# Performance work log

Measured on AMD Instinct MI355X. Metric: run time of the kernel, lower is better.

Reference implementation:

```python
import jax, jax.numpy as jnp
import numpy as np

N_NODES = 50000
N_EDGES = 800000
IN_F, HID, OUT_F = 256, 128, 8
N_LAYERS = 3
N_GRAPHS = 256
NEG_SLOPE = 0.2  # PyG GATConv default negative_slope


def setup_inputs() -> dict:
    key = jax.random.key(0)
    ks = jax.random.split(key, 16)
    inp = {
        "x": jax.random.normal(ks[0], (N_NODES, IN_F), dtype=jnp.float32),
        "edge_index": jax.random.randint(ks[1], (2, N_EDGES), 0, N_NODES, dtype=jnp.int64),
        "edge_attr": jax.random.normal(ks[2], (N_EDGES, 8), dtype=jnp.float32),
        "batch": jnp.sort(jax.random.randint(ks[3], (N_NODES,), 0, N_GRAPHS, dtype=jnp.int64)),
    }
    # Per-layer GATConv params (heads=1): lin weight, att_src, att_dst, bias.
    dims = [(IN_F, HID), (HID, HID), (HID, HID)]
    for l, (di, do) in enumerate(dims):
        s = 1.0 / np.sqrt(di)
        inp[f"W{l}"] = jax.random.uniform(ks[4 + l], (di, do), jnp.float32, -s, s)
        inp[f"a_src{l}"] = jax.random.normal(ks[7 + l], (do,), jnp.float32) * 0.1
        inp[f"a_dst{l}"] = jax.random.normal(ks[10 + l], (do,), jnp.float32) * 0.1
        inp[f"b{l}"] = jnp.zeros((do,), jnp.float32)
    s = 1.0 / np.sqrt(HID)
    inp["lin_w"] = jax.random.uniform(ks[13], (HID, OUT_F), jnp.float32, -s, s)
    inp["lin_b"] = jnp.zeros((OUT_F,), jnp.float32)
    return inp


def _segment_softmax(logits, seg, num_segments):
    m = jax.ops.segment_max(logits, seg, num_segments=num_segments)
    e = jnp.exp(logits - m[seg])
    s = jax.ops.segment_sum(e, seg, num_segments=num_segments)
    return e / s[seg]


def _gat_layer(x, src, dst, W, a_src, a_dst, b):
    h = x @ W                              # [N, H]
    alpha_s = h @ a_src                    # [N]
    alpha_d = h @ a_dst                    # [N]
    logits = jax.nn.leaky_relu(alpha_s[src] + alpha_d[dst], NEG_SLOPE)  # [E]
    alpha = _segment_softmax(logits, dst, N_NODES)                      # [E]
    out = jax.ops.segment_sum(alpha[:, None] * h[src], dst, num_segments=N_NODES)
    return out + b


def reference(x, edge_index, edge_attr, batch,
              W0, a_src0, a_dst0, b0,
              W1, a_src1, a_dst1, b1,
              W2, a_src2, a_dst2, b2,
              lin_w, lin_b):
    src, dst = edge_index[0], edge_index[1]
    # is_edge_attr=False: edge_attr unused, matching the else-branch.
    h = _gat_layer(x, src, dst, W0, a_src0, a_dst0, b0)
    h = jax.nn.relu(h)
    h = _gat_layer(h, src, dst, W1, a_src1, a_dst1, b1)
    h = jax.nn.relu(h)
    h = _gat_layer(h, src, dst, W2, a_src2, a_dst2, b2)  # last layer: no relu
    # global_mean_pool
    sums = jax.ops.segment_sum(h, batch, num_segments=N_GRAPHS)
    cnt = jax.ops.segment_sum(jnp.ones((N_NODES,), h.dtype), batch, num_segments=N_GRAPHS)
    pooled = sums / jnp.maximum(cnt, 1.0)[:, None]
    # Dropout is identity in eval mode.
    return pooled @ lin_w + lin_b  # logits [G, OUT_F]
```

## Files before the change

kernel.cpp:

```cpp
#include <hip/hip_runtime.h>
#include <cstdint>
#include <cstddef>

#define N_NODES_C  50000
#define N_EDGES_C  800000
#define IN_F_C     256
#define HID_C      128
#define N_GRAPHS_C 256
#define NEG_SLOPE_C 0.2f
#define SCAN_NB    ((N_NODES_C + 255) / 256)
#define POOL_SPLIT 8

typedef _Float16 f16x8 __attribute__((ext_vector_type(8)));
typedef float    f32x4 __attribute__((ext_vector_type(4)));

__global__ void hist_kernel(const int* __restrict__ dst, int* __restrict__ deg, int E) {
    int e = blockIdx.x * blockDim.x + threadIdx.x;
    if (e < E) atomicAdd(&deg[dst[e]], 1);
}

__global__ __launch_bounds__(256) void scan1_kernel(const int* __restrict__ deg,
                                                    int* __restrict__ bsum, int n) {
    int i = blockIdx.x * 256 + threadIdx.x;
    int lane = threadIdx.x & 63;
    int w = threadIdx.x >> 6;
    int v = (i < n) ? deg[i] : 0;
    #pragma unroll
    for (int off = 32; off >= 1; off >>= 1) v += __shfl_xor(v, off);
    __shared__ int ws_[4];
    if (lane == 0) ws_[w] = v;
    __syncthreads();
    if (threadIdx.x == 0) bsum[blockIdx.x] = ws_[0] + ws_[1] + ws_[2] + ws_[3];
}

__global__ __launch_bounds__(256) void scan2_kernel(int* __restrict__ bsum, int nb) {
    int t = threadIdx.x;
    int lane = t & 63;
    int w = t >> 6;
    int orig = (t < nb) ? bsum[t] : 0;
    int v = orig;
    #pragma unroll
    for (int off = 1; off < 64; off <<= 1) {
        int u = __shfl_up(v, off);
        if (lane >= off) v += u;
    }
    __shared__ int wsum[4];
    if (lane == 63) wsum[w] = v;
    __syncthreads();
    int add = 0;
    for (int i = 0; i < w; ++i) add += wsum[i];
    if (t < nb) bsum[t] = v + add - orig;
}

__global__ __launch_bounds__(256) void scan3_kernel(const int* __restrict__ deg,
                                                    const int* __restrict__ boff,
                                                    int* __restrict__ row_start,
                                                    int* __restrict__ cursor, int n) {
    int i = blockIdx.x * 256 + threadIdx.x;
    int lane = threadIdx.x & 63;
    int w = threadIdx.x >> 6;
    int d = (i < n) ? deg[i] : 0;
    int v = d;
    #pragma unroll
    for (int off = 1; off < 64; off <<= 1) {
        int u = __shfl_up(v, off);
        if (lane >= off) v += u;
    }
    __shared__ int wsum[4];
    if (lane == 63) wsum[w] = v;
    __syncthreads();
    int add = boff[blockIdx.x];
    for (int k = 0; k < w; ++k) add += wsum[k];
    int excl = v - d + add;
    if (i < n) {
        row_start[i] = excl;
        cursor[i] = excl;
        if (i == n - 1) row_start[n] = excl + d;
    }
}

__global__ void scatter_kernel(const int* __restrict__ src, const int* __restrict__ dst, int E,
                               int* __restrict__ cursor, int* __restrict__ csr_src) {
    int e = blockIdx.x * blockDim.x + threadIdx.x;
    if (e < E) {
        int pos = atomicAdd(&cursor[dst[e]], 1);
        csr_src[pos] = src[e];
    }
}

__global__ void convert_w_kernel(const float* __restrict__ W,
                                 _Float16* __restrict__ wt_hi,
                                 _Float16* __restrict__ wt_lo, int K) {
    int id = blockIdx.x * 256 + threadIdx.x;
    if (id >= K * 128) return;
    int c = id & 127;
    int k = id >> 7;
    float w = W[(size_t)k * 128 + c];
    _Float16 h = (_Float16)w;
    _Float16 l = (_Float16)(w - (float)h);
    wt_hi[(size_t)c * K + k] = h;
    wt_lo[(size_t)c * K + k] = l;
}

template <int K, bool RELU>
__global__ __launch_bounds__(256) void gemm_mfma_kernel(
    const float* __restrict__ X,
    const _Float16* __restrict__ WTh, const _Float16* __restrict__ WTl,
    const float* __restrict__ a_src, const float* __restrict__ a_dst,
    _Float16* __restrict__ Hh, float* __restrict__ alpha_s, float* __restrict__ alpha_d,
    int n_rows)
{
    constexpr int NS = K / 32;
    __shared__ _Float16 XsH[2][64 * 32];
    __shared__ _Float16 XsL[2][64 * 32];
    __shared__ float aps[4][64];
    __shared__ float apd[4][64];

    const int t = threadIdx.x;
    const int row0 = blockIdx.x * 64;
    const int lane = t & 63;
    const int wv = t >> 6;
    const int l15 = lane & 15;
    const int l4 = lane >> 4;
    const int wcol = wv * 32;

    const int sr = t >> 2;
    const int skg = t & 3;
    const int sgrow = row0 + sr;
    const int sslot = skg ^ (sr & 3);
    const int sldsoff = sr * 32 + sslot * 8;
    const bool srow_ok = (sgrow < n_rows);
    const float* __restrict__ srowp = X + (size_t)sgrow * K + skg * 8;

    f32x4 acc[4][2];
    #pragma unroll
    for (int mt = 0; mt < 4; ++mt)
        #pragma unroll
        for (int nt = 0; nt < 2; ++nt)
            acc[mt][nt] = (f32x4){0.f, 0.f, 0.f, 0.f};

    {
        float4 xa = make_float4(0.f, 0.f, 0.f, 0.f), xb = xa;
        if (srow_ok) {
            xa = *reinterpret_cast<const float4*>(srowp);
            xb = *reinterpret_cast<const float4*>(srowp + 4);
        }
        float v[8] = {xa.x, xa.y, xa.z, xa.w, xb.x, xb.y, xb.z, xb.w};
        f16x8 hi, lo;
        #pragma unroll
        for (int i = 0; i < 8; ++i) {
            float x = v[i];
            if (RELU) x = fmaxf(x, 0.f);
            _Float16 h = (_Float16)x;
            hi[i] = h;
            lo[i] = (_Float16)(x - (float)h);
        }
        *reinterpret_cast<f16x8*>(&XsH[0][sldsoff]) = hi;
        *reinterpret_cast<f16x8*>(&XsL[0][sldsoff]) = lo;
    }
    __syncthreads();

    int cur = 0;
    for (int step = 0; step < NS; ++step) {
        const int k0 = step * 32;
        float4 nxa = make_float4(0.f, 0.f, 0.f, 0.f), nxb = nxa;
        const bool hasNext = (step + 1 < NS);
        if (hasNext && srow_ok) {
            nxa = *reinterpret_cast<const float4*>(srowp + k0 + 32);
            nxb = *reinterpret_cast<const float4*>(srowp + k0 + 36);
        }
        f16x8 bh[2], bl[2];
        #pragma unroll
        for (int nt = 0; nt < 2; ++nt) {
            const size_t bo = (size_t)(wcol + nt * 16 + l15) * K + k0 + l4 * 8;
            bh[nt] = *reinterpret_cast<const f16x8*>(WTh + bo);
            bl[nt] = *reinterpret_cast<const f16x8*>(WTl + bo);
        }
        const int aslot = l4 ^ (l15 & 3);
        f16x8 ah[4], al[4];
        #pragma unroll
        for (int mt = 0; mt < 4; ++mt) {
            const int off = (mt * 16 + l15) * 32 + aslot * 8;
            ah[mt] = *reinterpret_cast<const f16x8*>(&XsH[cur][off]);
            al[mt] = *reinterpret_cast<const f16x8*>(&XsL[cur][off]);
        }
        #pragma unroll
        for (int mt = 0; mt < 4; ++mt)
            #pragma unroll
            for (int nt = 0; nt < 2; ++nt) {
                acc[mt][nt] = __builtin_amdgcn_mfma_f32_16x16x32_f16(ah[mt], bh[nt], acc[mt][nt], 0, 0, 0);
                acc[mt][nt] = __builtin_amdgcn_mfma_f32_16x16x32_f16(ah[mt], bl[nt], acc[mt][nt], 0, 0, 0);
                acc[mt][nt] = __builtin_amdgcn_mfma_f32_16x16x32_f16(al[mt], bh[nt], acc[mt][nt], 0, 0, 0);
            }
        if (hasNext) {
            float v[8] = {nxa.x, nxa.y, nxa.z, nxa.w, nxb.x, nxb.y, nxb.z, nxb.w};
            f16x8 hi, lo;
            #pragma unroll
            for (int i = 0; i < 8; ++i) {
                float x = v[i];
                if (RELU) x = fmaxf(x, 0.f);
                _Float16 h = (_Float16)x;
                hi[i] = h;
                lo[i] = (_Float16)(x - (float)h);
            }
            *reinterpret_cast<f16x8*>(&XsH[cur ^ 1][sldsoff]) = hi;
            *reinterpret_cast<f16x8*>(&XsL[cur ^ 1][sldsoff]) = lo;
        }
        __syncthreads();
        cur ^= 1;
    }

    const float as0 = a_src[wcol + l15];
    const float as1 = a_src[wcol + 16 + l15];
    const float ad0 = a_dst[wcol + l15];
    const float ad1 = a_dst[wcol + 16 + l15];

    #pragma unroll
    for (int mt = 0; mt < 4; ++mt) {
        #pragma unroll
        for (int reg = 0; reg < 4; ++reg) {
            const int lrow = mt * 16 + l4 * 4 + reg;
            const int grow = row0 + lrow;
            if (grow < n_rows) {
                Hh[(size_t)grow * 128 + wcol + l15]      = (_Float16)acc[mt][0][reg];
                Hh[(size_t)grow * 128 + wcol + 16 + l15] = (_Float16)acc[mt][1][reg];
            }
            float s = acc[mt][0][reg] * as0 + acc[mt][1][reg] * as1;
            float d = acc[mt][0][reg] * ad0 + acc[mt][1][reg] * ad1;
            #pragma unroll
            for (int off = 8; off >= 1; off >>= 1) {
                s += __shfl_xor(s, off);
                d += __shfl_xor(d, off);
            }
            if (l15 == 0) {
                aps[wv][lrow] = s;
                apd[wv][lrow] = d;
            }
        }
    }
    __syncthreads();
    if (t < 64) {
        const int grow = row0 + t;
        if (grow < n_rows)
            alpha_s[grow] = aps[0][t] + aps[1][t] + aps[2][t] + aps[3][t];
    } else if (t < 128) {
        const int tt = t - 64;
        const int grow = row0 + tt;
        if (grow < n_rows)
            alpha_d[grow] = apd[0][tt] + apd[1][tt] + apd[2][tt] + apd[3][tt];
    }
}

__global__ __launch_bounds__(256) void aggregate_kernel(
    const _Float16* __restrict__ Hh, const float* __restrict__ alpha_s,
    const float* __restrict__ alpha_d, const int* __restrict__ row_start,
    const int* __restrict__ csr_src, const float* __restrict__ bias,
    float* __restrict__ OUT, int n_nodes)
{
    int wid = (blockIdx.x * blockDim.x + threadIdx.x) >> 6;
    int lane = threadIdx.x & 63;
    if (wid >= n_nodes) return;

    int e0 = row_start[wid], e1 = row_start[wid + 1];
    float ad = alpha_d[wid];

    const int grp = lane >> 4;
    const int l16 = lane & 15;
    const _Float16* __restrict__ Hc = Hh + l16 * 8;

    float S = 0.f;
    float accA[8], accB[8], accC[8], accD[8];
    #pragma unroll
    for (int q = 0; q < 8; ++q) { accA[q] = 0.f; accB[q] = 0.f; accC[q] = 0.f; accD[q] = 0.f; }

    for (int base = e0; base < e1; base += 64) {
        int e = base + lane;
        float w = 0.f;
        int s = 0;
        if (e < e1) {
            s = csr_src[e];
            float z = alpha_s[s] + ad;
            z = (z >= 0.f) ? z : NEG_SLOPE_C * z;
            w = __expf(z);
        }
        float ws = w;
        #pragma unroll
        for (int off = 32; off >= 1; off >>= 1) ws += __shfl_xor(ws, off);
        S += ws;
        int cnt = min(64, e1 - base);

        for (int jj = 0; jj < cnt; jj += 16) {
            int i0 = jj + grp;
            int i1 = jj + 4 + grp;
            int i2 = jj + 8 + grp;
            int i3 = jj + 12 + grp;
            float w0 = __shfl(w, i0 & 63);
            int   s0 = __shfl(s, i0 & 63);
            float w1 = __shfl(w, i1 & 63);
            int   s1 = __shfl(s, i1 & 63);
            float w2 = __shfl(w, i2 & 63);
            int   s2 = __shfl(s, i2 & 63);
            float w3 = __shfl(w, i3 & 63);
            int   s3 = __shfl(s, i3 & 63);
            w0 = (i0 < cnt) ? w0 : 0.f;
            w1 = (i1 < cnt) ? w1 : 0.f;
            w2 = (i2 < cnt) ? w2 : 0.f;
            w3 = (i3 < cnt) ? w3 : 0.f;
            f16x8 h0 = *reinterpret_cast<const f16x8*>(Hc + (size_t)s0 * 128);
            f16x8 h1 = *reinterpret_cast<const f16x8*>(Hc + (size_t)s1 * 128);
            f16x8 h2 = *reinterpret_cast<const f16x8*>(Hc + (size_t)s2 * 128);
            f16x8 h3 = *reinterpret_cast<const f16x8*>(Hc + (size_t)s3 * 128);
            #pragma unroll
            for (int q = 0; q < 8; ++q) accA[q] = fmaf(w0, (float)h0[q], accA[q]);
            #pragma unroll
            for (int q = 0; q < 8; ++q) accB[q] = fmaf(w1, (float)h1[q], accB[q]);
            #pragma unroll
            for (int q = 0; q < 8; ++q) accC[q] = fmaf(w2, (float)h2[q], accC[q]);
            #pragma unroll
            for (int q = 0; q < 8; ++q) accD[q] = fmaf(w3, (float)h3[q], accD[q]);
        }
    }

    float acc[8];
    #pragma unroll
    for (int q = 0; q < 8; ++q) acc[q] = (accA[q] + accB[q]) + (accC[q] + accD[q]);
    #pragma unroll
    for (int q = 0; q < 8; ++q) {
        acc[q] += __shfl_xor(acc[q], 16);
        acc[q] += __shfl_xor(acc[q], 32);
    }

    float inv = (e1 > e0) ? (1.f / S) : 0.f;
    if (grp == 0) {
        float4 b0 = *reinterpret_cast<const float4*>(bias + l16 * 8);
        float4 b1 = *reinterpret_cast<const float4*>(bias + l16 * 8 + 4);
        float4 o0, o1;
        o0.x = acc[0] * inv + b0.x;
        o0.y = acc[1] * inv + b0.y;
        o0.z = acc[2] * inv + b0.z;
        o0.w = acc[3] * inv + b0.w;
        o1.x = acc[4] * inv + b1.x;
        o1.y = acc[5] * inv + b1.y;
        o1.z = acc[6] * inv + b1.z;
        o1.w = acc[7] * inv + b1.w;
        *reinterpret_cast<float4*>(OUT + (size_t)wid * 128 + l16 * 8)     = o0;
        *reinterpret_cast<float4*>(OUT + (size_t)wid * 128 + l16 * 8 + 4) = o1;
    }
}

__global__ void graph_ranges_kernel(const int* __restrict__ batch, int n_nodes,
                                    int n_graphs, int* __restrict__ gstart) {
    int g = blockIdx.x * blockDim.x + threadIdx.x;
    if (g > n_graphs) return;
    int lo = 0, hi = n_nodes;
    while (lo < hi) {
        int mid = (lo + hi) >> 1;
        if (batch[mid] < g) lo = mid + 1; else hi = mid;
    }
    gstart[g] = lo;
}

__global__ __launch_bounds__(128) void pool_partial_kernel(
    const float* __restrict__ X, const int* __restrict__ gstart,
    float* __restrict__ partial)
{
    int g = blockIdx.x >> 3;
    int split = blockIdx.x & 7;
    int c = threadIdx.x;
    int s = gstart[g], e = gstart[g + 1];
    int len = e - s;
    int i0 = s + (len * split) / POOL_SPLIT;
    int i1 = s + (len * (split + 1)) / POOL_SPLIT;
    float acc = 0.f;
    for (int i = i0; i < i1; ++i) acc += X[(size_t)i * 128 + c];
    partial[(size_t)blockIdx.x * 128 + c] = acc;
}

__global__ __launch_bounds__(128) void pool_final_kernel(
    const float* __restrict__ partial, const int* __restrict__ gstart,
    const float* __restrict__ lin_w, const float* __restrict__ lin_b,
    float* __restrict__ out)
{
    int g = blockIdx.x;
    int c = threadIdx.x;
    float acc = 0.f;
    #pragma unroll
    for (int sp = 0; sp < POOL_SPLIT; ++sp)
        acc += partial[(size_t)(g * POOL_SPLIT + sp) * 128 + c];
    float cnt = (float)(gstart[g + 1] - gstart[g]);
    float pooled = acc / fmaxf(cnt, 1.0f);
    __shared__ float p[128];
    p[c] = pooled;
    __syncthreads();
    if (c < 8) {
        float o = lin_b[c];
        for (int k = 0; k < 128; ++k) o += p[k] * lin_w[k * 8 + c];
        out[g * 8 + c] = o;
    }
}

extern "C" void kernel_launch(void* const* d_in, const int* in_sizes, int n_in,
                              void* d_out, int out_size, void* d_ws, size_t ws_size,
                              hipStream_t stream)
{
    const float* x     = (const float*)d_in[0];
    const int*   ei    = (const int*)d_in[1];
    const int*   batch = (const int*)d_in[3];
    const float* W[3]   = {(const float*)d_in[4],  (const float*)d_in[8],  (const float*)d_in[12]};
    const float* asr[3] = {(const float*)d_in[5],  (const float*)d_in[9],  (const float*)d_in[13]};
    const float* adt[3] = {(const float*)d_in[6],  (const float*)d_in[10], (const float*)d_in[14]};
    const float* bia[3] = {(const float*)d_in[7],  (const float*)d_in[11], (const float*)d_in[15]};
    const float* lin_w = (const float*)d_in[16];
    const float* lin_b = (const float*)d_in[17];
    float* out = (float*)d_out;

    char* ws = (char*)d_ws;
    size_t off = 0;
    auto carve = [&](size_t bytes) {
        void* p = ws + off;
        off = (off + bytes + 255) & ~(size_t)255;
        return p;
    };
    _Float16* Hh    = (_Float16*)carve((size_t)N_NODES_C * 128 * 2);
    float* bufB     = (float*)carve((size_t)N_NODES_C * 128 * 4);
    float* alpha_s  = (float*)carve((size_t)N_NODES_C * 4);
    float* alpha_d  = (float*)carve((size_t)N_NODES_C * 4);
    int*   deg      = (int*)carve((size_t)N_NODES_C * 4);
    int*   row_start= (int*)carve((size_t)(N_NODES_C + 1) * 4);
    int*   cursor   = (int*)carve((size_t)N_NODES_C * 4);
    int*   csr_src  = (int*)carve((size_t)N_EDGES_C * 4);
    int*   gstart   = (int*)carve((size_t)(N_GRAPHS_C + 1) * 4);
    int*   bsum     = (int*)carve((size_t)SCAN_NB * 4);
    float* ppart    = (float*)carve((size_t)N_GRAPHS_C * POOL_SPLIT * 128 * 4);
    _Float16* wt_h[3];
    _Float16* wt_l[3];
    wt_h[0] = (_Float16*)carve((size_t)128 * 256 * 2);
    wt_l[0] = (_Float16*)carve((size_t)128 * 256 * 2);
    wt_h[1] = (_Float16*)carve((size_t)128 * 128 * 2);
    wt_l[1] = (_Float16*)carve((size_t)128 * 128 * 2);
    wt_h[2] = (_Float16*)carve((size_t)128 * 128 * 2);
    wt_l[2] = (_Float16*)carve((size_t)128 * 128 * 2);

    const int* src = ei;
    const int* dst = ei + N_EDGES_C;

    hipMemsetAsync(deg, 0, (size_t)N_NODES_C * 4, stream);
    hist_kernel<<<(N_EDGES_C + 255) / 256, 256, 0, stream>>>(dst, deg, N_EDGES_C);
    scan1_kernel<<<SCAN_NB, 256, 0, stream>>>(deg, bsum, N_NODES_C);
    scan2_kernel<<<1, 256, 0, stream>>>(bsum, SCAN_NB);
    scan3_kernel<<<SCAN_NB, 256, 0, stream>>>(deg, bsum, row_start, cursor, N_NODES_C);
    scatter_kernel<<<(N_EDGES_C + 255) / 256, 256, 0, stream>>>(src, dst, N_EDGES_C,
                                                                cursor, csr_src);
    graph_ranges_kernel<<<2, 256, 0, stream>>>(batch, N_NODES_C, N_GRAPHS_C, gstart);
    convert_w_kernel<<<(256 * 128 + 255) / 256, 256, 0, stream>>>(W[0], wt_h[0], wt_l[0], 256);
    convert_w_kernel<<<(128 * 128 + 255) / 256, 256, 0, stream>>>(W[1], wt_h[1], wt_l[1], 128);
    convert_w_kernel<<<(128 * 128 + 255) / 256, 256, 0, stream>>>(W[2], wt_h[2], wt_l[2], 128);

    const int gemm_grid = (N_NODES_C + 63) / 64;
    const int agg_grid  = (N_NODES_C + 3) / 4;

    gemm_mfma_kernel<IN_F_C, false><<<gemm_grid, 256, 0, stream>>>(
        x, wt_h[0], wt_l[0], asr[0], adt[0], Hh, alpha_s, alpha_d, N_NODES_C);
    aggregate_kernel<<<agg_grid, 256, 0, stream>>>(
        Hh, alpha_s, alpha_d, row_start, csr_src, bia[0], bufB, N_NODES_C);

    gemm_mfma_kernel<HID_C, true><<<gemm_grid, 256, 0, stream>>>(
        bufB, wt_h[1], wt_l[1], asr[1], adt[1], Hh, alpha_s, alpha_d, N_NODES_C);
    aggregate_kernel<<<agg_grid, 256, 0, stream>>>(
        Hh, alpha_s, alpha_d, row_start, csr_src, bia[1], bufB, N_NODES_C);

    gemm_mfma_kernel<HID_C, true><<<gemm_grid, 256, 0, stream>>>(
        bufB, wt_h[2], wt_l[2], asr[2], adt[2], Hh, alpha_s, alpha_d, N_NODES_C);
    aggregate_kernel<<<agg_grid, 256, 0, stream>>>(
        Hh, alpha_s, alpha_d, row_start, csr_src, bia[2], bufB, N_NODES_C);

    pool_partial_kernel<<<N_GRAPHS_C * POOL_SPLIT, 128, 0, stream>>>(bufB, gstart, ppart);
    pool_final_kernel<<<N_GRAPHS_C, 128, 0, stream>>>(ppart, gstart, lin_w, lin_b, out);
}
```

Measured before the change: 445.8 us.

## Record per-edge rank in histogram and scatter CSR by destination buckets

The histogram kernel now keeps the value returned by its atomic increment as each edge's rank within its destination row. This removes the second atomic pass over a cursor array in the scatter step. The scatter kernel then writes csr_src[row_start[d]+rank[e]] with no atomics. It is split into 8 destination buckets across edge chunks so that each block's writes stay in a narrower address range. The cost is an extra 800K-int rank array, and every edge's dst is read 8 times across the buckets.

```diff
diff --git a/kernel.cpp b/kernel.cpp
--- a/kernel.cpp
+++ b/kernel.cpp
@@ -10,13 +10,16 @@
 #define NEG_SLOPE_C 0.2f
 #define SCAN_NB    ((N_NODES_C + 255) / 256)
 #define POOL_SPLIT 8
+#define SCAT_BUCKETS 8
+#define SCAT_CHUNKS  256
 
 typedef _Float16 f16x8 __attribute__((ext_vector_type(8)));
 typedef float    f32x4 __attribute__((ext_vector_type(4)));
 
-__global__ void hist_kernel(const int* __restrict__ dst, int* __restrict__ deg, int E) {
+__global__ void hist_rank_kernel(const int* __restrict__ dst, int* __restrict__ deg,
+                                 int* __restrict__ rank, int E) {
     int e = blockIdx.x * blockDim.x + threadIdx.x;
-    if (e < E) atomicAdd(&deg[dst[e]], 1);
+    if (e < E) rank[e] = atomicAdd(&deg[dst[e]], 1);
 }
 
 __global__ __launch_bounds__(256) void scan1_kernel(const int* __restrict__ deg,
@@ -54,8 +57,7 @@
 
 __global__ __launch_bounds__(256) void scan3_kernel(const int* __restrict__ deg,
                                                     const int* __restrict__ boff,
-                                                    int* __restrict__ row_start,
-                                                    int* __restrict__ cursor, int n) {
+                                                    int* __restrict__ row_start, int n) {
     int i = blockIdx.x * 256 + threadIdx.x;
     int lane = threadIdx.x & 63;
     int w = threadIdx.x >> 6;
@@ -74,17 +76,28 @@
     int excl = v - d + add;
     if (i < n) {
         row_start[i] = excl;
-        cursor[i] = excl;
         if (i == n - 1) row_start[n] = excl + d;
     }
 }
 
-__global__ void scatter_kernel(const int* __restrict__ src, const int* __restrict__ dst, int E,
-                               int* __restrict__ cursor, int* __restrict__ csr_src) {
-    int e = blockIdx.x * blockDim.x + threadIdx.x;
-    if (e < E) {
-        int pos = atomicAdd(&cursor[dst[e]], 1);
-        csr_src[pos] = src[e];
+__global__ __launch_bounds__(256) void scatter_bucket_kernel(
+    const int* __restrict__ src, const int* __restrict__ dst,
+    const int* __restrict__ rank, const int* __restrict__ row_start,
+    int* __restrict__ csr_src, int E)
+{
+    const int bucket = blockIdx.x & (SCAT_BUCKETS - 1);
+    const int chunk  = blockIdx.x / SCAT_BUCKETS;
+    constexpr int NPB = (N_NODES_C + SCAT_BUCKETS - 1) / SCAT_BUCKETS;
+    const int lo = bucket * NPB;
+    const int hi = min(lo + NPB, N_NODES_C);
+    const int per = (E + SCAT_CHUNKS - 1) / SCAT_CHUNKS;
+    const int e0 = chunk * per;
+    const int e1 = min(e0 + per, E);
+    for (int e = e0 + (int)threadIdx.x; e < e1; e += 256) {
+        int d = dst[e];
+        if (d >= lo && d < hi) {
+            csr_src[row_start[d] + rank[e]] = src[e];
+        }
     }
 }
 
@@ -427,7 +440,7 @@
     float* alpha_d  = (float*)carve((size_t)N_NODES_C * 4);
     int*   deg      = (int*)carve((size_t)N_NODES_C * 4);
     int*   row_start= (int*)carve((size_t)(N_NODES_C + 1) * 4);
-    int*   cursor   = (int*)carve((size_t)N_NODES_C * 4);
+    int*   rank     = (int*)carve((size_t)N_EDGES_C * 4);
     int*   csr_src  = (int*)carve((size_t)N_EDGES_C * 4);
     int*   gstart   = (int*)carve((size_t)(N_GRAPHS_C + 1) * 4);
     int*   bsum     = (int*)carve((size_t)SCAN_NB * 4);
@@ -445,12 +458,12 @@
     const int* dst = ei + N_EDGES_C;
 
     hipMemsetAsync(deg, 0, (size_t)N_NODES_C * 4, stream);
-    hist_kernel<<<(N_EDGES_C + 255) / 256, 256, 0, stream>>>(dst, deg, N_EDGES_C);
+    hist_rank_kernel<<<(N_EDGES_C + 255) / 256, 256, 0, stream>>>(dst, deg, rank, N_EDGES_C);
     scan1_kernel<<<SCAN_NB, 256, 0, stream>>>(deg, bsum, N_NODES_C);
     scan2_kernel<<<1, 256, 0, stream>>>(bsum, SCAN_NB);
-    scan3_kernel<<<SCAN_NB, 256, 0, stream>>>(deg, bsum, row_start, cursor, N_NODES_C);
-    scatter_kernel<<<(N_EDGES_C + 255) / 256, 256, 0, stream>>>(src, dst, N_EDGES_C,
-                                                                cursor, csr_src);
+    scan3_kernel<<<SCAN_NB, 256, 0, stream>>>(deg, bsum, row_start, N_NODES_C);
+    scatter_bucket_kernel<<<SCAT_BUCKETS * SCAT_CHUNKS, 256, 0, stream>>>(
+        src, dst, rank, row_start, csr_src, N_EDGES_C);
     graph_ranges_kernel<<<2, 256, 0, stream>>>(batch, N_NODES_C, N_GRAPHS_C, gstart);
     convert_w_kernel<<<(256 * 128 + 255) / 256, 256, 0, stream>>>(W[0], wt_h[0], wt_l[0], 256);
     convert_w_kernel<<<(128 * 128 + 255) / 256, 256, 0, stream>>>(W[1], wt_h[1], wt_l[1], 128);
```

Result: faster. 407.5 us (-8.6%).
